# Optimization experiments

Hardware: AMD Instinct MI355X
Metric: run time of the kernel (lower is better)

The kernel has to match this reference:

```python
import jax, jax.numpy as jnp
import numpy as np
from jax import lax

# ---- constants mirroring Prediction.__init__ kwargs ----
INP = 608
NUM_CLASSES = 20
ALPHA, BETA = 1.0, 0.5
OBJ_T, CONF_T, LOC_T = 0.6, 0.05, 0.5
NMS_T, SIZE_T, SIGMA = 0.1, 0.0, 0.5
TOP_K = 8
M_CAND = 256          # fixed-size candidate cap for jit-compatible NMS
NEG = -1e9            # sentinel for masked scores
ANCHORS = [[(116, 90), (156, 198), (373, 326)],
           [(30, 61), (62, 45), (59, 119)],
           [(10, 13), (16, 30), (33, 23)]]


def _decode(pred, anchors):
    """pred: (B, A, G, G, 6+C) raw level output -> decoded flat tensors."""
    B, A, G, _, C = pred.shape
    stride = INP // G
    xy = jax.nn.sigmoid(pred[..., 0:2])
    g = jnp.arange(G, dtype=pred.dtype)
    gx, gy = jnp.meshgrid(g, g)                      # gx[i,j]=j, gy[i,j]=i (np.meshgrid 'xy')
    off = jnp.stack([gx, gy], axis=-1)[None, None]   # (1,1,G,G,2)
    xy = ALPHA * xy - 0.5 * (ALPHA - 1.0) + off
    anc = jnp.asarray(anchors, dtype=pred.dtype) / stride  # (A,2) scaled to grid units
    wh = jnp.exp(pred[..., 2:4]) * anc[None, :, None, None, :]
    box = jnp.concatenate([xy, wh], axis=-1) * stride       # back to pixel units
    obj = jax.nn.sigmoid(pred[..., 4])
    loc = jax.nn.sigmoid(pred[..., 5])
    clsp = jax.nn.softmax(pred[..., 6:], axis=-1)
    N = A * G * G
    return (box.reshape(B, N, 4), obj.reshape(B, N),
            loc.reshape(B, N), clsp.reshape(B, N, NUM_CLASSES))


def _soft_nms(boxes, s0, cls):
    """Per-image Gaussian soft-NMS (class-aware), +1 pixel IoU convention as in bbox_iou.
    boxes: (M,4) xyxy, s0: (M,) scores (NEG for invalid), cls: (M,) int. Returns kept mask."""
    M = s0.shape[0]

    def step(carry, _):
        s, kept = carry
        j = jnp.argmax(s)
        do = s[j] >= NMS_T
        kept = kept | ((jnp.arange(M) == j) & do)
        bj = boxes[j]
        ix1 = jnp.maximum(bj[0], boxes[:, 0]); iy1 = jnp.maximum(bj[1], boxes[:, 1])
        ix2 = jnp.minimum(bj[2], boxes[:, 2]); iy2 = jnp.minimum(bj[3], boxes[:, 3])
        inter = jnp.maximum(ix2 - ix1 + 1.0, 0.0) * jnp.maximum(iy2 - iy1 + 1.0, 0.0)
        a1 = (bj[2] - bj[0] + 1.0) * (bj[3] - bj[1] + 1.0)
        a2 = (boxes[:, 2] - boxes[:, 0] + 1.0) * (boxes[:, 3] - boxes[:, 1] + 1.0)
        iou = inter / (a1 + a2 - inter + 1e-16)
        decay = jnp.exp(-(iou * iou) / SIGMA)
        s_new = jnp.where(cls == cls[j], s * decay, s).at[j].set(NEG)
        s = jnp.where(do, s_new, s)
        return (s, kept), None

    (_, kept), _ = lax.scan(step, (s0, jnp.zeros(M, dtype=bool)), None, length=M)
    return kept


def _forward(pred_l0, pred_l1, pred_l2):
    parts = [_decode(p, a) for p, a in zip([pred_l0, pred_l1, pred_l2], ANCHORS)]
    box = jnp.concatenate([p[0] for p in parts], axis=1)   # (B,N,4) xywh
    obj = jnp.concatenate([p[1] for p in parts], axis=1)
    loc = jnp.concatenate([p[2] for p in parts], axis=1)
    clsp = jnp.concatenate([p[3] for p in parts], axis=1)

    cx, cy, w, h = box[..., 0], box[..., 1], box[..., 2], box[..., 3]
    x1 = jnp.clip(cx - w / 2, 0.0, INP); y1 = jnp.clip(cy - h / 2, 0.0, INP)
    x2 = jnp.clip(cx + w / 2, 0.0, INP); y2 = jnp.clip(cy + h / 2, 0.0, INP)
    boxes = jnp.stack([x1, y1, x2, y2], axis=-1)            # (B,N,4) xyxy, clamped

    cls_conf = jnp.max(clsp, axis=-1)
    cls_id = jnp.argmax(clsp, axis=-1)
    area = (x2 - x1) * (y2 - y1)
    valid = ((obj >= OBJ_T) & (area >= INP * INP * SIZE_T)
             & (obj * cls_conf >= CONF_T) & (loc >= LOC_T))
    score = (obj * cls_conf) ** BETA * loc ** (1.0 - BETA)
    masked = jnp.where(valid, score, NEG)

    # fixed-size candidate set per image (descending-score sort + cap)
    vals, idx = lax.top_k(masked, M_CAND)                   # (B,M)
    cboxes = jnp.take_along_axis(boxes, idx[..., None], axis=1)
    ccls = jnp.take_along_axis(cls_id, idx, axis=1)
    s0 = jnp.where(vals > NEG / 2, vals, NEG)

    kept = jax.vmap(_soft_nms)(cboxes, s0, ccls)            # (B,M) bool

    # keep_top_k: top_k among kept, ranked by ORIGINAL (pre-decay) score
    fscore = jnp.where(kept, vals, NEG)
    fvals, fidx = lax.top_k(fscore, TOP_K)                  # (B,TOP_K)
    fboxes = jnp.take_along_axis(cboxes, fidx[..., None], axis=1)
    fcls = jnp.take_along_axis(ccls, fidx, axis=1)
    row = jnp.concatenate([fboxes, fvals[..., None],
                           fcls[..., None].astype(fboxes.dtype)], axis=-1)  # (B,K,6)
    ok = fvals > NEG / 2
    return jnp.where(ok[..., None], row, 0.0)


def setup_inputs() -> dict:
    key = jax.random.key(0)
    k0, k1, k2 = jax.random.split(key, 3)
    return {
        "pred_l0": jax.random.normal(k0, (64, 3, 19, 19, 26), dtype=jnp.float32),
        "pred_l1": jax.random.normal(k1, (64, 3, 38, 38, 26), dtype=jnp.float32),
        "pred_l2": jax.random.normal(k2, (64, 3, 76, 76, 26), dtype=jnp.float32),
    }


def reference(pred_l0, pred_l1, pred_l2):
    return _forward(pred_l0, pred_l1, pred_l2)
```

## Files before the change

kernel.cpp:

```cpp
#include <hip/hip_runtime.h>
#include <climits>
#include <cstdint>

constexpr int kB  = 64;
constexpr int kG0 = 19, kG1 = 38, kG2 = 76;
constexpr int kN0 = 3 * kG0 * kG0;
constexpr int kN1 = 3 * kG1 * kG1;
constexpr int kN2 = 3 * kG2 * kG2;
constexpr int kN  = kN0 + kN1 + kN2;
constexpr int kNP = kN + 1;
constexpr int kM  = 256;
constexpr int kTopK = 8;
constexpr float kNEG = -1e9f;
constexpr int kHB = 4096;

constexpr int kT0 = 5, kT1 = 17, kT2 = 68;
constexpr int kTilesPerImg = kT0 + kT1 + kT2;
constexpr int kGridScore = kB * kTilesPerImg;

__constant__ float c_anchors[3][3][2] = {
    {{116.f, 90.f}, {156.f, 198.f}, {373.f, 326.f}},
    {{30.f, 61.f},  {62.f, 45.f},   {59.f, 119.f}},
    {{10.f, 13.f},  {16.f, 30.f},   {33.f, 23.f}},
};

typedef float f4_t __attribute__((ext_vector_type(4)));

__device__ __forceinline__ float fexpf(float x) { return __expf(x); }
__device__ __forceinline__ float frcpf(float x) { return __builtin_amdgcn_rcpf(x); }
__device__ __forceinline__ float fsigm(float x) { return frcpf(1.0f + __expf(-x)); }

__device__ __forceinline__ float2 nt_load_f2(const float2* p) {
  unsigned long long v = __builtin_nontemporal_load((const unsigned long long*)p);
  union { unsigned long long u; float2 f; } c; c.u = v; return c.f;
}
__device__ __forceinline__ f4_t nt_load_f4(const f4_t* p) {
  return __builtin_nontemporal_load(p);
}

__device__ __forceinline__ unsigned score_to_key(float s) {
  unsigned fb = __float_as_uint(s);
  unsigned m = (fb & 0x80000000u) ? 0xFFFFFFFFu : 0x80000000u;
  return fb ^ m;
}
__device__ __forceinline__ float key_to_score(unsigned k) {
  unsigned fb = (k & 0x80000000u) ? (k ^ 0x80000000u) : ~k;
  return __uint_as_float(fb);
}

__device__ __forceinline__ const float* cell_ptr(
    const float* p0, const float* p1, const float* p2, int b, int n,
    int& lvl, int& a, int& gi, int& gj, float& stride) {
  const float* src; int G, m;
  if (n < kN0)            { src = p0; G = kG0; lvl = 0; m = n;             stride = 32.f; }
  else if (n < kN0 + kN1) { src = p1; G = kG1; lvl = 1; m = n - kN0;       stride = 16.f; }
  else                    { src = p2; G = kG2; lvl = 2; m = n - kN0 - kN1; stride = 8.f; }
  int gg = G * G;
  a = m / gg;
  int r = m - a * gg;
  gi = r / G;
  gj = r - gi * G;
  return src + (size_t)((((b * 3 + a) * G + gi) * G + gj)) * 26;
}

__device__ __forceinline__ void waveArgmax(float& v, int& i) {
  #pragma unroll
  for (int off = 1; off < 64; off <<= 1) {
    float ov = __shfl_xor(v, off);
    int oi = __shfl_xor(i, off);
    if (ov > v || (ov == v && oi < i)) { v = ov; i = oi; }
  }
}
__device__ __forceinline__ float waveMax(float v) {
  #pragma unroll
  for (int off = 1; off < 64; off <<= 1) v = fmaxf(v, __shfl_xor(v, off));
  return v;
}
__device__ __forceinline__ float sel4f(const float a[4], int q) {
  float r = a[0];
  r = (q == 1) ? a[1] : r;
  r = (q == 2) ? a[2] : r;
  r = (q == 3) ? a[3] : r;
  return r;
}
__device__ __forceinline__ int sel4i(const int a[4], int q) {
  int r = a[0];
  r = (q == 1) ? a[1] : r;
  r = (q == 2) ? a[2] : r;
  r = (q == 3) ? a[3] : r;
  return r;
}

__global__ __launch_bounds__(256) void score_kernel(
    const float* __restrict__ p0, const float* __restrict__ p1, const float* __restrict__ p2,
    unsigned* __restrict__ keys)
{
  __shared__ float lds[256 * 26];

  int t = threadIdx.x;
  int tileId = (int)blockIdx.x;
  int b = tileId / kTilesPerImg;
  int r = tileId - b * kTilesPerImg;
  const float* slab; int NL, lvlOff, tile;
  if (r < kT0)            { slab = p0; NL = kN0; lvlOff = 0;         tile = r; }
  else if (r < kT0 + kT1) { slab = p1; NL = kN1; lvlOff = kN0;       tile = r - kT0; }
  else                    { slab = p2; NL = kN2; lvlOff = kN0 + kN1; tile = r - kT0 - kT1; }
  int cellBase = tile * 256;
  int nc = min(256, NL - cellBase);
  const float* g = slab + ((size_t)b * NL + cellBase) * 26;
  int nf = nc * 26;

  if ((((uintptr_t)g) & 15) == 0) {
    int n4 = nf >> 2;
    f4_t* d4 = (f4_t*)lds;
    #pragma unroll
    for (int k = 0; k < 7; ++k) {
      int i = t + k * 256;
      if (i < n4) d4[i] = nt_load_f4((const f4_t*)g + i);
    }
    if ((nf & 3) && t == 0) {
      ((float2*)lds)[n4 << 1] = nt_load_f2((const float2*)g + (n4 << 1));
    }
  } else {
    int n2 = nf >> 1;
    float2* d2 = (float2*)lds;
    #pragma unroll
    for (int k = 0; k < 13; ++k) {
      int i = t + k * 256;
      if (i < n2) d2[i] = nt_load_f2((const float2*)g + i);
    }
  }
  __syncthreads();

  if (t < nc) {
    const float2* c2 = (const float2*)&lds[t * 26];
    float2 ol = c2[2];
    float obj = fsigm(ol.x);
    float loc = fsigm(ol.y);
    float tch[20];
    #pragma unroll
    for (int q = 0; q < 10; ++q) { float2 v = c2[3 + q]; tch[2*q] = v.x; tch[2*q+1] = v.y; }
    float lm = tch[0];
    #pragma unroll
    for (int c = 1; c < 20; ++c) lm = fmaxf(lm, tch[c]);
    float se = 0.f;
    #pragma unroll
    for (int c = 0; c < 20; ++c) se += fexpf(tch[c] - lm);
    float cls_conf = frcpf(se);
    float conf = obj * cls_conf;
    float masked = (obj >= 0.6f && loc >= 0.5f && conf >= 0.05f)
                   ? sqrtf(conf) * sqrtf(loc) : kNEG;
    keys[(size_t)b * kNP + lvlOff + cellBase + t] = score_to_key(masked);
  }
}

__device__ __forceinline__ void findThresholdBin(
    const int* hist, int NB, int needed,
    int& outB, int& outCumAbove, int& outTotal,
    int* shWave, int* shOut)
{
  int tid = threadIdx.x, lane = tid & 63, w = tid >> 6;
  if (tid == 0) { shOut[0] = -1; shOut[1] = 0; }
  int ipt = (NB + 511) / 512;
  int base = tid * ipt;
  int csum = 0;
  for (int i = 0; i < ipt; ++i) { int bn = base + i; if (bn < NB) csum += hist[bn]; }
  int v = csum;
  #pragma unroll
  for (int off = 1; off < 64; off <<= 1) {
    int tv = __shfl_down(v, off);
    if (lane + off < 64) v += tv;
  }
  if (lane == 0) shWave[w] = v;
  __syncthreads();
  int above = 0, total = 0;
  #pragma unroll
  for (int q = 0; q < 8; ++q) {
    int wt = shWave[q];
    total += wt;
    if (q > w) above += wt;
  }
  int S = v + above;
  if (S >= needed && S - csum < needed) {
    int running = S - csum;
    for (int i = ipt - 1; i >= 0; --i) {
      int bn = base + i; if (bn >= NB) continue;
      int c = hist[bn];
      if (running + c >= needed) { shOut[0] = bn; shOut[1] = running; break; }
      running += c;
    }
  }
  __syncthreads();
  outB = shOut[0]; outCumAbove = shOut[1]; outTotal = total;
  __syncthreads();
}

constexpr int kNV4 = kN / 4;
constexpr int kTail = kN - kNV4*4;

__global__ __launch_bounds__(512) void select_nms_kernel(
    const unsigned* __restrict__ keys,
    const float* __restrict__ p0, const float* __restrict__ p1, const float* __restrict__ p2,
    float* __restrict__ out)
{
  int b = blockIdx.x, tid = threadIdx.x;
  const unsigned* kk = keys + (size_t)b * kNP;
  const uint4* kk4 = (const uint4*)kk;
  const unsigned keyNEG = score_to_key(kNEG);

  constexpr int kPool = 4096;
  __shared__ int hist[kHB];
  __shared__ int shWave[8], shOut[2];
  __shared__ int ciL[kM];
  __shared__ unsigned ckL[kM];
  __shared__ unsigned pk[kPool];
  __shared__ int piA[kPool];
  __shared__ int eqI[256];
  __shared__ int sCnt, eqCnt, sTie;

  for (int i = tid; i < kHB; i += 512) hist[i] = 0;
  __syncthreads();
  for (int x = tid; x < kNV4; x += 512) {
    uint4 v = kk4[x];
    if (v.x >= 0x80000000u) atomicAdd(&hist[v.x >> 20], 1);
    if (v.y >= 0x80000000u) atomicAdd(&hist[v.y >> 20], 1);
    if (v.z >= 0x80000000u) atomicAdd(&hist[v.z >> 20], 1);
    if (v.w >= 0x80000000u) atomicAdd(&hist[v.w >> 20], 1);
  }
  if (tid < kTail) {
    unsigned k = kk[kNV4 * 4 + tid];
    if (k >= 0x80000000u) atomicAdd(&hist[k >> 20], 1);
  }
  __syncthreads();
  int B, cumAbove1, total1;
  findThresholdBin(hist, kHB, kM, B, cumAbove1, total1, shWave, shOut);

  if (tid == 0) { sCnt = 0; eqCnt = 0; sTie = 0; }
  for (int i = tid; i < kHB; i += 512) hist[i] = 0;
  __syncthreads();

  if (total1 < kM) {
    for (int x = tid; x < kNV4; x += 512) {
      uint4 v = kk4[x];
      int i4 = x * 4;
      unsigned kv[4] = {v.x, v.y, v.z, v.w};
      #pragma unroll
      for (int e = 0; e < 4; ++e) {
        unsigned k = kv[e];
        if (k & 0x80000000u) { int p = atomicAdd(&sCnt, 1); ciL[p] = i4 + e; ckL[p] = k; }
      }
    }
    if (tid < kTail) {
      int x = kNV4 * 4 + tid;
      unsigned k = kk[x];
      if (k & 0x80000000u) { int p = atomicAdd(&sCnt, 1); ciL[p] = x; ckL[p] = k; }
    }
    __syncthreads();
    if (tid >= total1 && tid < kM) { ciL[tid] = -1; ckL[tid] = keyNEG; }
    __syncthreads();
  } else {
    unsigned uB = (unsigned)B;
    for (int x = tid; x < kNV4; x += 512) {
      uint4 v = kk4[x];
      int i4 = x * 4;
      unsigned kv[4] = {v.x, v.y, v.z, v.w};
      #pragma unroll
      for (int e = 0; e < 4; ++e) {
        unsigned k = kv[e];
        unsigned hi = k >> 20;
        if (hi > uB) { int p = atomicAdd(&sCnt, 1); ciL[p] = i4 + e; ckL[p] = k; }
        else if (hi == uB) {
          int p = atomicAdd(&eqCnt, 1);
          if (p < kPool) { pk[p] = k; piA[p] = i4 + e; }
          atomicAdd(&hist[(k >> 8) & 0xFFFu], 1);
        }
      }
    }
    if (tid < kTail) {
      int x = kNV4 * 4 + tid;
      unsigned k = kk[x];
      unsigned hi = k >> 20;
      if (hi > uB) { int p = atomicAdd(&sCnt, 1); ciL[p] = x; ckL[p] = k; }
      else if (hi == uB) {
        int p = atomicAdd(&eqCnt, 1);
        if (p < kPool) { pk[p] = k; piA[p] = x; }
        atomicAdd(&hist[(k >> 8) & 0xFFFu], 1);
      }
    }
    __syncthreads();

    int needed = kM - cumAbove1;
    int pc = eqCnt;

    if (pc == needed) {
      if (tid < pc) { ciL[cumAbove1 + tid] = piA[tid]; ckL[cumAbove1 + tid] = pk[tid]; }
      __syncthreads();
    } else if (pc <= kPool) {
      int B2, cA2, tot2;
      findThresholdBin(hist, kHB, needed, B2, cA2, tot2, shWave, shOut);
      for (int i = tid; i < 256; i += 512) hist[i] = 0;
      __syncthreads();
      for (int i = tid; i < pc; i += 512) {
        unsigned k = pk[i];
        int mid = (int)((k >> 8) & 0xFFFu);
        if (mid > B2) { int p = atomicAdd(&sCnt, 1); ciL[p] = piA[i]; ckL[p] = k; }
        else if (mid == B2) atomicAdd(&hist[k & 0xFFu], 1);
      }
      __syncthreads();
      int needed3 = needed - cA2;
      int B3, cA3, tot3;
      findThresholdBin(hist, 256, needed3, B3, cA3, tot3, shWave, shOut);
      for (int i = tid; i < pc; i += 512) {
        unsigned k = pk[i];
        int mid = (int)((k >> 8) & 0xFFFu);
        if (mid == B2) {
          int lo = (int)(k & 0xFFu);
          if (lo > B3) { int p = atomicAdd(&sCnt, 1); ciL[p] = piA[i]; ckL[p] = k; }
          else if (lo == B3) { int p = atomicAdd(&sTie, 1); if (p < 256) eqI[p] = piA[i]; }
        }
      }
      __syncthreads();
      int needed4 = needed3 - cA3;
      unsigned exactKey = (uB << 20) | ((unsigned)B2 << 8) | (unsigned)B3;
      int nt_ = sTie;
      if (nt_ == needed4) {
        if (tid < needed4) {
          int base0 = kM - needed4;
          ciL[base0 + tid] = eqI[tid]; ckL[base0 + tid] = exactKey;
        }
      } else if (tid == 0) {
        int base0 = kM - needed4; int lastI = -1;
        for (int q = 0; q < needed4; ++q) {
          int mv = INT_MAX;
          for (int x = 0; x < pc; ++x) {
            if (pk[x] == exactKey) { int ix = piA[x]; if (ix > lastI && ix < mv) mv = ix; }
          }
          ciL[base0 + q] = mv; ckL[base0 + q] = exactKey; lastI = mv;
        }
      }
      __syncthreads();
    } else {
      if (tid == 0) {
        int base0 = sCnt;
        unsigned lastK = 0xFFFFFFFFu; int lastI = INT_MAX;
        for (int q = 0; q < needed; ++q) {
          unsigned bk = 0u; int bi2 = -1;
          for (int x = 0; x < kN; ++x) {
            unsigned k = kk[x];
            if ((k >> 20) != uB) continue;
            if (k > lastK || (k == lastK && x <= lastI)) continue;
            if (bi2 < 0 || k > bk || (k == bk && x < bi2)) { bk = k; bi2 = x; }
          }
          ciL[base0 + q] = bi2; ckL[base0 + q] = bk; lastK = bk; lastI = bi2;
        }
      }
      __syncthreads();
    }
  }

  if (tid >= 64) return;
  int lane = tid;

  float x1[4], y1[4], x2[4], y2[4], val[4], s[4];
  int cls[4];
  bool kept[4];

  #pragma unroll
  for (int q = 0; q < 4; ++q) {
    int slot = q * 64 + lane;
    int n = ciL[slot];
    float sc = key_to_score(ckL[slot]);
    kept[q] = false;
    x1[q] = y1[q] = x2[q] = y2[q] = 0.f;
    cls[q] = 0; val[q] = sc; s[q] = sc;
    if (n >= 0) {
      int lvl, a, gi, gj; float stride;
      const float* p = cell_ptr(p0, p1, p2, b, n, lvl, a, gi, gj, stride);
      const float2* r2 = (const float2*)p;
      float2 c01 = r2[0], c23 = r2[1];
      float cx = (fsigm(c01.x) + (float)gj) * stride;
      float cy = (fsigm(c01.y) + (float)gi) * stride;
      float w = fexpf(c23.x) * c_anchors[lvl][a][0];
      float h = fexpf(c23.y) * c_anchors[lvl][a][1];
      x1[q] = fminf(fmaxf(cx - 0.5f * w, 0.f), 608.f);
      y1[q] = fminf(fmaxf(cy - 0.5f * h, 0.f), 608.f);
      x2[q] = fminf(fmaxf(cx + 0.5f * w, 0.f), 608.f);
      y2[q] = fminf(fmaxf(cy + 0.5f * h, 0.f), 608.f);
      float lm = -3.4e38f; int mc = 0;
      #pragma unroll
      for (int j = 3; j < 13; ++j) {
        float2 v = r2[j];
        int c0 = 2 * (j - 3);
        if (v.x > lm) { lm = v.x; mc = c0; }
        if (v.y > lm) { lm = v.y; mc = c0 + 1; }
      }
      cls[q] = mc;
    }
  }

  float top8[8];
  #pragma unroll
  for (int i = 0; i < 8; ++i) top8[i] = kNEG;
  int keptCount = 0;

  for (int it = 0; it < kM; ++it) {
    float bv = s[0]; int bq = 0;
    #pragma unroll
    for (int q = 1; q < 4; ++q) if (s[q] > bv) { bv = s[q]; bq = q; }
    int bi = bq * 64 + lane;
    waveArgmax(bv, bi);
    if (bv < 0.1f) break;

    int wlane = bi & 63, wq = bi >> 6;
    float jx1 = __shfl(sel4f(x1, wq), wlane);
    float jy1 = __shfl(sel4f(y1, wq), wlane);
    float jx2 = __shfl(sel4f(x2, wq), wlane);
    float jy2 = __shfl(sel4f(y2, wq), wlane);
    float jval = __shfl(sel4f(val, wq), wlane);
    int   cj  = __shfl(sel4i(cls, wq), wlane);

    float a1 = (jx2 - jx1 + 1.0f) * (jy2 - jy1 + 1.0f);
    #pragma unroll
    for (int q = 0; q < 4; ++q) {
      if (cls[q] == cj) {
        float ix1 = fmaxf(jx1, x1[q]), iy1 = fmaxf(jy1, y1[q]);
        float ix2 = fminf(jx2, x2[q]), iy2 = fminf(jy2, y2[q]);
        float inter = fmaxf(ix2 - ix1 + 1.0f, 0.0f) * fmaxf(iy2 - iy1 + 1.0f, 0.0f);
        float a2 = (x2[q] - x1[q] + 1.0f) * (y2[q] - y1[q] + 1.0f);
        float iou = inter / (a1 + a2 - inter + 1e-16f);
        s[q] *= fexpf(-(iou * iou) * 2.0f);
      }
      if (bi == q * 64 + lane) { kept[q] = true; s[q] = kNEG; }
    }

    float v = jval;
    #pragma unroll
    for (int i = 0; i < 8; ++i) { float m = fmaxf(top8[i], v); v = fminf(top8[i], v); top8[i] = m; }
    ++keptCount;
    if (keptCount >= kTopK) {
      float am = kNEG;
      #pragma unroll
      for (int q = 0; q < 4; ++q) if (s[q] >= 0.1f) am = fmaxf(am, val[q]);
      am = waveMax(am);
      if (am < top8[7]) break;
    }
  }

  float f[4];
  #pragma unroll
  for (int q = 0; q < 4; ++q) f[q] = kept[q] ? val[q] : kNEG;
  for (int k = 0; k < kTopK; ++k) {
    float bv = f[0]; int bq = 0;
    #pragma unroll
    for (int q = 1; q < 4; ++q) if (f[q] > bv) { bv = f[q]; bq = q; }
    int bi = bq * 64 + lane;
    waveArgmax(bv, bi);
    int wlane = bi & 63, wq = bi >> 6;
    if (lane == wlane) {
      float* o = out + (size_t)(b * kTopK + k) * 6;
      if (bv > kNEG * 0.5f) {
        o[0] = sel4f(x1, wq); o[1] = sel4f(y1, wq);
        o[2] = sel4f(x2, wq); o[3] = sel4f(y2, wq);
        o[4] = sel4f(val, wq); o[5] = (float)sel4i(cls, wq);
      } else {
        o[0] = 0.f; o[1] = 0.f; o[2] = 0.f; o[3] = 0.f; o[4] = 0.f; o[5] = 0.f;
      }
    }
    #pragma unroll
    for (int q = 0; q < 4; ++q) if (bi == q * 64 + lane) f[q] = kNEG;
  }
}

extern "C" void kernel_launch(void* const* d_in, const int* in_sizes, int n_in,
                              void* d_out, int out_size, void* d_ws, size_t ws_size,
                              hipStream_t stream) {
  const float* p0 = (const float*)d_in[0];
  const float* p1 = (const float*)d_in[1];
  const float* p2 = (const float*)d_in[2];
  float* out = (float*)d_out;

  unsigned* keys = (unsigned*)d_ws;

  score_kernel<<<kGridScore, 256, 0, stream>>>(p0, p1, p2, keys);
  select_nms_kernel<<<kB, 512, 0, stream>>>(keys, p0, p1, p2, out);
}
```

Measured before the change: 224.2 us.

## Compact valid candidates per tile in score kernel, select from compacted list

The score kernel now uses a wavefront ballot and prefix count to write only valid (key, index) pairs into a per-tile compacted list, with a per-tile count, instead of writing a dense key array that includes invalid entries. The select kernel builds segment offsets from the tile counts, stages the compacted entries into LDS when they fit, and runs the radix-threshold passes over only the valid entries. This is meant to cut the select kernel's full scans of roughly 22k keys per image, done by only 64 blocks. The cost is extra per-block synchronisation in the score kernel, a larger workspace, and a binary search over segments for each entry when staging or when falling back to global memory.

```diff
diff --git a/kernel.cpp b/kernel.cpp
--- a/kernel.cpp
+++ b/kernel.cpp
@@ -8,7 +8,6 @@
 constexpr int kN1 = 3 * kG1 * kG1;
 constexpr int kN2 = 3 * kG2 * kG2;
 constexpr int kN  = kN0 + kN1 + kN2;
-constexpr int kNP = kN + 1;
 constexpr int kM  = 256;
 constexpr int kTopK = 8;
 constexpr float kNEG = -1e9f;
@@ -93,9 +92,10 @@
 
 __global__ __launch_bounds__(256) void score_kernel(
     const float* __restrict__ p0, const float* __restrict__ p1, const float* __restrict__ p2,
-    unsigned* __restrict__ keys)
+    uint2* __restrict__ list, int* __restrict__ tcnt)
 {
   __shared__ float lds[256 * 26];
+  __shared__ int wcnt[4];
 
   int t = threadIdx.x;
   int tileId = (int)blockIdx.x;
@@ -132,6 +132,8 @@
   }
   __syncthreads();
 
+  bool valid = false;
+  unsigned key = 0;
   if (t < nc) {
     const float2* c2 = (const float2*)&lds[t * 26];
     float2 ol = c2[2];
@@ -148,10 +150,23 @@
     for (int c = 0; c < 20; ++c) se += fexpf(tch[c] - lm);
     float cls_conf = frcpf(se);
     float conf = obj * cls_conf;
-    float masked = (obj >= 0.6f && loc >= 0.5f && conf >= 0.05f)
-                   ? sqrtf(conf) * sqrtf(loc) : kNEG;
-    keys[(size_t)b * kNP + lvlOff + cellBase + t] = score_to_key(masked);
-  }
+    valid = (obj >= 0.6f && loc >= 0.5f && conf >= 0.05f);
+    if (valid) key = score_to_key(sqrtf(conf) * sqrtf(loc));
+  }
+
+  unsigned long long m = __ballot(valid);
+  int lane = t & 63, w = t >> 6;
+  if (lane == 0) wcnt[w] = (int)__popcll(m);
+  __syncthreads();
+  int base = 0;
+  #pragma unroll
+  for (int q = 0; q < 4; ++q) if (q < w) base += wcnt[q];
+  int off = base + (int)__popcll(m & ((1ull << lane) - 1ull));
+  if (valid) {
+    uint2 e; e.x = key; e.y = (unsigned)(lvlOff + cellBase + t);
+    list[(size_t)tileId * 256 + off] = e;
+  }
+  if (t == 0) tcnt[tileId] = wcnt[0] + wcnt[1] + wcnt[2] + wcnt[3];
 }
 
 __device__ __forceinline__ void findThresholdBin(
@@ -195,167 +210,119 @@
   __syncthreads();
 }
 
-constexpr int kNV4 = kN / 4;
-constexpr int kTail = kN - kNV4*4;
-
+constexpr int kCap = 6144;
 __global__ __launch_bounds__(512) void select_nms_kernel(
-    const unsigned* __restrict__ keys,
+    const uint2* __restrict__ list, const int* __restrict__ tcnt,
     const float* __restrict__ p0, const float* __restrict__ p1, const float* __restrict__ p2,
     float* __restrict__ out)
 {
   int b = blockIdx.x, tid = threadIdx.x;
-  const unsigned* kk = keys + (size_t)b * kNP;
-  const uint4* kk4 = (const uint4*)kk;
   const unsigned keyNEG = score_to_key(kNEG);
 
-  constexpr int kPool = 4096;
   __shared__ int hist[kHB];
   __shared__ int shWave[8], shOut[2];
   __shared__ int ciL[kM];
   __shared__ unsigned ckL[kM];
-  __shared__ unsigned pk[kPool];
-  __shared__ int piA[kPool];
+  __shared__ unsigned eK[kCap];
+  __shared__ unsigned short eI[kCap];
+  __shared__ int segOff[kTilesPerImg + 1];
   __shared__ int eqI[256];
-  __shared__ int sCnt, eqCnt, sTie;
-
-  for (int i = tid; i < kHB; i += 512) hist[i] = 0;
-  __syncthreads();
-  for (int x = tid; x < kNV4; x += 512) {
-    uint4 v = kk4[x];
-    if (v.x >= 0x80000000u) atomicAdd(&hist[v.x >> 20], 1);
-    if (v.y >= 0x80000000u) atomicAdd(&hist[v.y >> 20], 1);
-    if (v.z >= 0x80000000u) atomicAdd(&hist[v.z >> 20], 1);
-    if (v.w >= 0x80000000u) atomicAdd(&hist[v.w >> 20], 1);
-  }
-  if (tid < kTail) {
-    unsigned k = kk[kNV4 * 4 + tid];
-    if (k >= 0x80000000u) atomicAdd(&hist[k >> 20], 1);
-  }
-  __syncthreads();
-  int B, cumAbove1, total1;
-  findThresholdBin(hist, kHB, kM, B, cumAbove1, total1, shWave, shOut);
-
-  if (tid == 0) { sCnt = 0; eqCnt = 0; sTie = 0; }
-  for (int i = tid; i < kHB; i += 512) hist[i] = 0;
-  __syncthreads();
-
-  if (total1 < kM) {
-    for (int x = tid; x < kNV4; x += 512) {
-      uint4 v = kk4[x];
-      int i4 = x * 4;
-      unsigned kv[4] = {v.x, v.y, v.z, v.w};
-      #pragma unroll
-      for (int e = 0; e < 4; ++e) {
-        unsigned k = kv[e];
-        if (k & 0x80000000u) { int p = atomicAdd(&sCnt, 1); ciL[p] = i4 + e; ckL[p] = k; }
-      }
-    }
-    if (tid < kTail) {
-      int x = kNV4 * 4 + tid;
-      unsigned k = kk[x];
-      if (k & 0x80000000u) { int p = atomicAdd(&sCnt, 1); ciL[p] = x; ckL[p] = k; }
-    }
-    __syncthreads();
-    if (tid >= total1 && tid < kM) { ciL[tid] = -1; ckL[tid] = keyNEG; }
+  __shared__ int sCnt, sTie;
+
+  if (tid < kTilesPerImg) segOff[tid + 1] = tcnt[b * kTilesPerImg + tid];
+  if (tid == 0) segOff[0] = 0;
+  __syncthreads();
+  if (tid == 0) { for (int s = 0; s < kTilesPerImg; ++s) segOff[s + 1] += segOff[s]; }
+  __syncthreads();
+  int total = segOff[kTilesPerImg];
+  bool inLds = (total <= kCap);
+
+  auto entryAt = [&](int i) -> uint2 {
+    if (inLds) { uint2 e; e.x = eK[i]; e.y = eI[i]; return e; }
+    int lo = 0, hi = kTilesPerImg - 1;
+    while (lo < hi) { int mid = (lo + hi + 1) >> 1; if (segOff[mid] <= i) lo = mid; else hi = mid - 1; }
+    return list[((size_t)b * kTilesPerImg + lo) * 256 + (i - segOff[lo])];
+  };
+
+  if (inLds) {
+    for (int i = tid; i < total; i += 512) {
+      int lo = 0, hi = kTilesPerImg - 1;
+      while (lo < hi) { int mid = (lo + hi + 1) >> 1; if (segOff[mid] <= i) lo = mid; else hi = mid - 1; }
+      uint2 e = list[((size_t)b * kTilesPerImg + lo) * 256 + (i - segOff[lo])];
+      eK[i] = e.x; eI[i] = (unsigned short)e.y;
+    }
+  }
+  if (tid == 0) { sCnt = 0; sTie = 0; }
+  __syncthreads();
+
+  if (total < kM) {
+    for (int i = tid; i < total; i += 512) { uint2 e = entryAt(i); ciL[i] = (int)e.y; ckL[i] = e.x; }
+    __syncthreads();
+    if (tid >= total && tid < kM) { ciL[tid] = -1; ckL[tid] = keyNEG; }
     __syncthreads();
   } else {
+    for (int i = tid; i < kHB; i += 512) hist[i] = 0;
+    __syncthreads();
+    for (int i = tid; i < total; i += 512) atomicAdd(&hist[entryAt(i).x >> 20], 1);
+    __syncthreads();
+    int B, cumAbove1, t1;
+    findThresholdBin(hist, kHB, kM, B, cumAbove1, t1, shWave, shOut);
     unsigned uB = (unsigned)B;
-    for (int x = tid; x < kNV4; x += 512) {
-      uint4 v = kk4[x];
-      int i4 = x * 4;
-      unsigned kv[4] = {v.x, v.y, v.z, v.w};
-      #pragma unroll
-      for (int e = 0; e < 4; ++e) {
-        unsigned k = kv[e];
-        unsigned hi = k >> 20;
-        if (hi > uB) { int p = atomicAdd(&sCnt, 1); ciL[p] = i4 + e; ckL[p] = k; }
-        else if (hi == uB) {
-          int p = atomicAdd(&eqCnt, 1);
-          if (p < kPool) { pk[p] = k; piA[p] = i4 + e; }
-          atomicAdd(&hist[(k >> 8) & 0xFFFu], 1);
+    for (int i = tid; i < kHB; i += 512) hist[i] = 0;
+    __syncthreads();
+
+    for (int i = tid; i < total; i += 512) {
+      uint2 e = entryAt(i);
+      unsigned hi = e.x >> 20;
+      if (hi > uB) { int p = atomicAdd(&sCnt, 1); ciL[p] = (int)e.y; ckL[p] = e.x; }
+      else if (hi == uB) atomicAdd(&hist[(e.x >> 8) & 0xFFFu], 1);
+    }
+    __syncthreads();
+    int needed = kM - cumAbove1;
+    int B2, cA2, t2;
+    findThresholdBin(hist, kHB, needed, B2, cA2, t2, shWave, shOut);
+    for (int i = tid; i < 256; i += 512) hist[i] = 0;
+    __syncthreads();
+
+    for (int i = tid; i < total; i += 512) {
+      uint2 e = entryAt(i);
+      if ((e.x >> 20) == uB) {
+        int mid = (int)((e.x >> 8) & 0xFFFu);
+        if (mid > B2) { int p = atomicAdd(&sCnt, 1); ciL[p] = (int)e.y; ckL[p] = e.x; }
+        else if (mid == B2) atomicAdd(&hist[e.x & 0xFFu], 1);
+      }
+    }
+    __syncthreads();
+    int needed3 = needed - cA2;
+    int B3, cA3, t3;
+    findThresholdBin(hist, 256, needed3, B3, cA3, t3, shWave, shOut);
+
+    for (int i = tid; i < total; i += 512) {
+      uint2 e = entryAt(i);
+      if ((e.x >> 20) == uB && (int)((e.x >> 8) & 0xFFFu) == B2) {
+        int lo = (int)(e.x & 0xFFu);
+        if (lo > B3) { int p = atomicAdd(&sCnt, 1); ciL[p] = (int)e.y; ckL[p] = e.x; }
+        else if (lo == B3) { int p = atomicAdd(&sTie, 1); if (p < 256) eqI[p] = (int)e.y; }
+      }
+    }
+    __syncthreads();
+    int needed4 = needed3 - cA3;
+    unsigned exactKey = (uB << 20) | ((unsigned)B2 << 8) | (unsigned)B3;
+    int ties = sTie;
+    if (ties == needed4) {
+      if (tid < needed4) { ciL[kM - needed4 + tid] = eqI[tid]; ckL[kM - needed4 + tid] = exactKey; }
+    } else if (tid == 0) {
+      int base0 = kM - needed4; int lastI = -1;
+      for (int q = 0; q < needed4; ++q) {
+        int mv = INT_MAX;
+        for (int i = 0; i < total; ++i) {
+          uint2 e = entryAt(i);
+          if (e.x == exactKey) { int ix = (int)e.y; if (ix > lastI && ix < mv) mv = ix; }
         }
-      }
-    }
-    if (tid < kTail) {
-      int x = kNV4 * 4 + tid;
-      unsigned k = kk[x];
-      unsigned hi = k >> 20;
-      if (hi > uB) { int p = atomicAdd(&sCnt, 1); ciL[p] = x; ckL[p] = k; }
-      else if (hi == uB) {
-        int p = atomicAdd(&eqCnt, 1);
-        if (p < kPool) { pk[p] = k; piA[p] = x; }
-        atomicAdd(&hist[(k >> 8) & 0xFFFu], 1);
-      }
-    }
-    __syncthreads();
-
-    int needed = kM - cumAbove1;
-    int pc = eqCnt;
-
-    if (pc == needed) {
-      if (tid < pc) { ciL[cumAbove1 + tid] = piA[tid]; ckL[cumAbove1 + tid] = pk[tid]; }
-      __syncthreads();
-    } else if (pc <= kPool) {
-      int B2, cA2, tot2;
-      findThresholdBin(hist, kHB, needed, B2, cA2, tot2, shWave, shOut);
-      for (int i = tid; i < 256; i += 512) hist[i] = 0;
-      __syncthreads();
-      for (int i = tid; i < pc; i += 512) {
-        unsigned k = pk[i];
-        int mid = (int)((k >> 8) & 0xFFFu);
-        if (mid > B2) { int p = atomicAdd(&sCnt, 1); ciL[p] = piA[i]; ckL[p] = k; }
-        else if (mid == B2) atomicAdd(&hist[k & 0xFFu], 1);
-      }
-      __syncthreads();
-      int needed3 = needed - cA2;
-      int B3, cA3, tot3;
-      findThresholdBin(hist, 256, needed3, B3, cA3, tot3, shWave, shOut);
-      for (int i = tid; i < pc; i += 512) {
-        unsigned k = pk[i];
-        int mid = (int)((k >> 8) & 0xFFFu);
-        if (mid == B2) {
-          int lo = (int)(k & 0xFFu);
-          if (lo > B3) { int p = atomicAdd(&sCnt, 1); ciL[p] = piA[i]; ckL[p] = k; }
-          else if (lo == B3) { int p = atomicAdd(&sTie, 1); if (p < 256) eqI[p] = piA[i]; }
-        }
-      }
-      __syncthreads();
-      int needed4 = needed3 - cA3;
-      unsigned exactKey = (uB << 20) | ((unsigned)B2 << 8) | (unsigned)B3;
-      int nt_ = sTie;
-      if (nt_ == needed4) {
-        if (tid < needed4) {
-          int base0 = kM - needed4;
-          ciL[base0 + tid] = eqI[tid]; ckL[base0 + tid] = exactKey;
-        }
-      } else if (tid == 0) {
-        int base0 = kM - needed4; int lastI = -1;
-        for (int q = 0; q < needed4; ++q) {
-          int mv = INT_MAX;
-          for (int x = 0; x < pc; ++x) {
-            if (pk[x] == exactKey) { int ix = piA[x]; if (ix > lastI && ix < mv) mv = ix; }
-          }
-          ciL[base0 + q] = mv; ckL[base0 + q] = exactKey; lastI = mv;
-        }
-      }
-      __syncthreads();
-    } else {
-      if (tid == 0) {
-        int base0 = sCnt;
-        unsigned lastK = 0xFFFFFFFFu; int lastI = INT_MAX;
-        for (int q = 0; q < needed; ++q) {
-          unsigned bk = 0u; int bi2 = -1;
-          for (int x = 0; x < kN; ++x) {
-            unsigned k = kk[x];
-            if ((k >> 20) != uB) continue;
-            if (k > lastK || (k == lastK && x <= lastI)) continue;
-            if (bi2 < 0 || k > bk || (k == bk && x < bi2)) { bk = k; bi2 = x; }
-          }
-          ciL[base0 + q] = bi2; ckL[base0 + q] = bk; lastK = bk; lastI = bi2;
-        }
-      }
-      __syncthreads();
-    }
+        ciL[base0 + q] = mv; ckL[base0 + q] = exactKey; lastI = mv;
+      }
+    }
+    __syncthreads();
   }
 
   if (tid >= 64) return;
@@ -479,8 +446,9 @@
   const float* p2 = (const float*)d_in[2];
   float* out = (float*)d_out;
 
-  unsigned* keys = (unsigned*)d_ws;
-
-  score_kernel<<<kGridScore, 256, 0, stream>>>(p0, p1, p2, keys);
-  select_nms_kernel<<<kB, 512, 0, stream>>>(keys, p0, p1, p2, out);
-}
+  uint2* list = (uint2*)d_ws;
+  int* tcnt = (int*)((char*)d_ws + (size_t)kB * kTilesPerImg * 256 * sizeof(uint2));
+
+  score_kernel<<<kGridScore, 256, 0, stream>>>(p0, p1, p2, list, tcnt);
+  select_nms_kernel<<<kB, 512, 0, stream>>>(list, tcnt, p0, p1, p2, out);
+}
```

Measured after the change: 233.5 us. 1.04x slower.
